# Performance work log

Measured on AMD Instinct MI355X. Metric: run time of the kernel, lower is better.

Reference implementation:

```python
import jax, jax.numpy as jnp
import numpy as np

N = 50000      # nodes
E = 800000     # edges (before self loops)
F_IN = 128     # input feature dim
H = 2          # attention heads
C = 64         # hidden channels per head (H*C = 128 = layer-2 input dim)
G = 64         # graphs in batch
OUT = 10       # out_channels
NEG_SLOPE = 0.2  # PyG GATConv default leaky relu slope


def setup_inputs() -> dict:
    key = jax.random.key(0)
    ks = jax.random.split(key, 16)
    sc = lambda f: np.float32(1.0 / np.sqrt(f))
    inp = {
        "x": jax.random.normal(ks[0], (N, F_IN), jnp.float32),
        "edge_index": jax.random.randint(ks[1], (2, E), 0, N, dtype=jnp.int32),
        "batch": jnp.sort(jax.random.randint(ks[2], (N,), 0, G, dtype=jnp.int32)),
        # GATConv layer 1 (lazy (-1,-1): separate src/dst projections)
        "Ws1": jax.random.normal(ks[3], (F_IN, H * C), jnp.float32) * sc(F_IN),
        "Wd1": jax.random.normal(ks[4], (F_IN, H * C), jnp.float32) * sc(F_IN),
        "as1": jax.random.normal(ks[5], (H, C), jnp.float32) * sc(C),
        "ad1": jax.random.normal(ks[6], (H, C), jnp.float32) * sc(C),
        "b1": jnp.zeros((H * C,), jnp.float32),
        # GATConv layer 2 (input dim = H*C = 128)
        "Ws2": jax.random.normal(ks[7], (H * C, H * C), jnp.float32) * sc(H * C),
        "Wd2": jax.random.normal(ks[8], (H * C, H * C), jnp.float32) * sc(H * C),
        "as2": jax.random.normal(ks[9], (H, C), jnp.float32) * sc(C),
        "ad2": jax.random.normal(ks[10], (H, C), jnp.float32) * sc(C),
        "b2": jnp.zeros((H * C,), jnp.float32),
        # final linear
        "Wl": jax.random.normal(ks[11], (H * C, OUT), jnp.float32) * sc(H * C),
        "bl": jnp.zeros((OUT,), jnp.float32),
    }
    return inp


def gat_conv(x, src, dst, Ws, Wd, att_s, att_d, b):
    # x: [N, F]; src/dst: [E'] (self loops already included)
    n = x.shape[0]
    xs = (x @ Ws).reshape(n, H, C)          # source-side projection
    xd = (x @ Wd).reshape(n, H, C)          # dest-side projection
    a_s = jnp.einsum('nhc,hc->nh', xs, att_s)   # [N, H]
    a_d = jnp.einsum('nhc,hc->nh', xd, att_d)   # [N, H]
    e = a_s[src] + a_d[dst]                      # [E', H]
    e = jnp.where(e > 0, e, NEG_SLOPE * e)       # leaky_relu
    # softmax over incoming edges per destination node (every node has a self loop)
    m = jax.ops.segment_max(e, dst, num_segments=n)
    ew = jnp.exp(e - m[dst])
    denom = jax.ops.segment_sum(ew, dst, num_segments=n)
    alpha = ew / denom[dst]                      # [E', H]
    out = jax.ops.segment_sum(alpha[:, :, None] * xs[src], dst, num_segments=n)
    return out.reshape(n, H * C) + b


def reference(x, edge_index, batch, Ws1, Wd1, as1, ad1, b1, Ws2, Wd2, as2, ad2, b2, Wl, bl):
    # add self loops once (add_self_loops=True)
    loops = jnp.arange(N, dtype=edge_index.dtype)
    src = jnp.concatenate([edge_index[0], loops])
    dst = jnp.concatenate([edge_index[1], loops])

    h = jax.nn.relu(gat_conv(x, src, dst, Ws1, Wd1, as1, ad1, b1))
    h = jax.nn.relu(gat_conv(h, src, dst, Ws2, Wd2, as2, ad2, b2))

    # global_mean_pool over batch vector
    sums = jax.ops.segment_sum(h, batch, num_segments=G)
    cnt = jax.ops.segment_sum(jnp.ones((N,), h.dtype), batch, num_segments=G)
    pooled = sums / jnp.maximum(cnt, 1.0)[:, None]

    # dropout(p=0.5) is identity in eval mode
    return pooled @ Wl + bl
```

## Files before the change

kernel.cpp:

```cpp
#include <hip/hip_runtime.h>
#include <hip/hip_bf16.h>

#define N_NODES 50000
#define N_EDGES 800000
#define EP (N_EDGES + N_NODES)
#define N_GRAPHS 64
#define F_DIM 128
#define OUT_DIM 10
#define NB 391
#define NREP 8
#define SUBCAP 384
#define EIDS_CAP 2560
#define SC_EDGES 4096
#define SC_BLOCKS ((N_EDGES + SC_EDGES - 1) / SC_EDGES)
#define POOL_CHUNK 128
#define POOL_BLOCKS ((N_NODES + POOL_CHUNK - 1) / POOL_CHUNK)

typedef __attribute__((ext_vector_type(8))) short short8;
typedef __attribute__((ext_vector_type(4))) float f32x4;

__device__ __forceinline__ unsigned int f2bf(float f) {
    unsigned int x; __builtin_memcpy(&x, &f, 4);
    return (x + 0x7fffu + ((x >> 16) & 1u)) >> 16;
}
__device__ __forceinline__ float bf2f(unsigned int u16) {
    unsigned int x = u16 << 16;
    float f; __builtin_memcpy(&f, &x, 4); return f;
}


__global__ __launch_bounds__(256) void prep_kernel(
    const float* __restrict__ W1, const float* __restrict__ W2,
    const float* __restrict__ Wd1, const float* __restrict__ ad1,
    const float* __restrict__ Wd2, const float* __restrict__ ad2,
    unsigned short* __restrict__ Wt1, unsigned short* __restrict__ Wt2,
    float* __restrict__ weffd1, float* __restrict__ weffd2,
    uint4* __restrict__ zero_bcur , uint4* __restrict__ zero_sums ) {
    int tid = blockIdx.x * 256 + threadIdx.x;
    if (tid < 782) zero_bcur[tid] = make_uint4(0, 0, 0, 0);
    else if (tid < 782 + 2048) zero_sums[tid - 782] = make_uint4(0, 0, 0, 0);
    if (tid < 512) {
        const float* Wd = (tid < 256) ? Wd1 : Wd2;
        const float* ad = (tid < 256) ? ad1 : ad2;
        float* wout = (tid < 256) ? weffd1 : weffd2;
        int i = tid & 255, f = i >> 1, h = i & 1;
        const float4* wr = (const float4*)(Wd + f * 128 + h * 64);
        const float4* av = (const float4*)(ad + h * 64);
        float s = 0.f;
        #pragma unroll
        for (int c = 0; c < 16; ++c) {
            float4 w = wr[c], a = av[c];
            s += w.x*a.x + w.y*a.y + w.z*a.z + w.w*a.w;
        }
        wout[f * 2 + h] = s;
    }
    const float* W = (tid < 16384) ? W1 : W2;
    unsigned short* Wt = (tid < 16384) ? Wt1 : Wt2;
    int i = tid & 16383;
    int k = i >> 7, nn = i & 127;
    Wt[nn * 128 + k] = (unsigned short)f2bf(W[i]);
}


__global__ __launch_bounds__(1024) void scatter_kernel(const int* __restrict__ ei,
                                                       int* __restrict__ bcursor,
                                                       unsigned int* __restrict__ recs) {
    __shared__ unsigned int srec[SC_EDGES];
    __shared__ int hist[NB], lcur[NB], gpos[NB];
    __shared__ int excl[512];
    int t = threadIdx.x;
    int base = blockIdx.x * SC_EDGES;
    int rep = blockIdx.x & (NREP - 1);
    for (int i = t; i < NB; i += 1024) { hist[i] = 0; lcur[i] = 0; }
    __syncthreads();
    unsigned int rec_[4]; int have[4];
    #pragma unroll
    for (int j = 0; j < 4; ++j) {
        int i = base + j * 1024 + t;
        have[j] = (i < N_EDGES);
        if (have[j]) {
            int src = ei[i], dst = ei[N_EDGES + i];
            int b = dst >> 7;
            rec_[j] = ((unsigned)b << 23) | ((unsigned)(dst & 127) << 16) | (unsigned)src;
            atomicAdd(&hist[b], 1);
        }
    }
    __syncthreads();
    if (t < 512) excl[t] = (t < NB) ? hist[t] : 0;
    __syncthreads();
    for (int off = 1; off < 512; off <<= 1) {
        int v = 0;
        if (t < 512 && t >= off) v = excl[t - off];
        __syncthreads();
        if (t < 512) excl[t] += v;
        __syncthreads();
    }
    if (t < NB && hist[t] > 0) gpos[t] = atomicAdd(&bcursor[rep * NB + t], hist[t]);
    __syncthreads();
    #pragma unroll
    for (int j = 0; j < 4; ++j) {
        if (have[j]) {
            int b = rec_[j] >> 23;
            int pos = atomicAdd(&lcur[b], 1);
            srec[(excl[b] - hist[b]) + pos] = rec_[j];
        }
    }
    __syncthreads();
    int cnt = N_EDGES - base; if (cnt > SC_EDGES) cnt = SC_EDGES;
    for (int i = t; i < cnt; i += 1024) {
        unsigned int rec = srec[i];
        int b = rec >> 23;
        int gp = gpos[b] + (i - (excl[b] - hist[b]));
        if (gp < SUBCAP)
            recs[((size_t)b * NREP + rep) * SUBCAP + gp] = rec & 0x7fffffu;
    }
}

__global__ __launch_bounds__(256) void bucketize_kernel(
    const unsigned int* __restrict__ recs, const int* __restrict__ bcursor,
    unsigned short* __restrict__ eids, int2* __restrict__ rsre, int n) {
    __shared__ int ssub[NREP + 1];
    __shared__ int hist[128], excl[128], cur[128];
    __shared__ unsigned int srec[EIDS_CAP];
    int b = blockIdx.x, t = threadIdx.x;
    int nvalid = n - b * 128; if (nvalid > 128) nvalid = 128;
    if (t < 128) { hist[t] = 0; cur[t] = 0; }
    if (t == 0) {
        int run = 0; ssub[0] = 0;
        for (int r = 0; r < NREP; ++r) {
            int c = bcursor[r * NB + b]; if (c > SUBCAP) c = SUBCAP;
            run += c; ssub[r + 1] = run;
        }
    }
    __syncthreads();
    int total = ssub[NREP];
    int maxsc = EIDS_CAP - 128;
    if (total > maxsc) total = maxsc;
    const unsigned int* rb = recs + (size_t)b * NREP * SUBCAP;
    for (int i = t; i < total; i += 256) {
        int r = 0;
        while (ssub[r + 1] <= i) ++r;
        unsigned int rec = rb[r * SUBCAP + (i - ssub[r])];
        srec[i] = rec;
        atomicAdd(&hist[(rec >> 16) & 127], 1);
    }
    __syncthreads();
    if (t < nvalid) hist[t] += 1;
    __syncthreads();
    if (t < 128) excl[t] = hist[t];
    __syncthreads();
    for (int off = 1; off < 128; off <<= 1) {
        int v = 0;
        if (t < 128 && t >= off) v = excl[t - off];
        __syncthreads();
        if (t < 128) excl[t] += v;
        __syncthreads();
    }
    int base2 = b * EIDS_CAP;
    if (t < nvalid) {
        int st = excl[t] - hist[t];
        rsre[b * 128 + t] = make_int2(base2 + st, base2 + excl[t]);
        eids[base2 + st] = (unsigned short)(b * 128 + t);
        cur[t] = 1;
    }
    __syncthreads();
    for (int i = t; i < total; i += 256) {
        unsigned int rec = srec[i];
        int dl = (rec >> 16) & 127;
        int pos = atomicAdd(&cur[dl], 1);
        eids[base2 + (excl[dl] - hist[dl]) + pos] = (unsigned short)(rec & 0xffffu);
    }
}


__global__ __launch_bounds__(256) void gemm_fused_f32a_kernel(
    const float* __restrict__ A, const unsigned short* __restrict__ Wt,
    const float* __restrict__ att_s, const float* __restrict__ weffd,
    unsigned short* __restrict__ C, float* __restrict__ a_s, float* __restrict__ a_d, int n) {
    int t = threadIdx.x;
    int l = t & 63;
    int quad = l >> 4, lr = l & 15;
    int m0 = blockIdx.x * 64 + (t >> 6) * 16;
    int arow = m0 + lr; if (arow >= n) arow = n - 1;

    short8 afrag[4];
    float pd0 = 0.f, pd1 = 0.f;
    const float2* wd2 = (const float2*)weffd;
    #pragma unroll
    for (int kb = 0; kb < 4; ++kb) {
        const float4* ap = (const float4*)(A + (size_t)arow * 128 + kb * 32 + quad * 8);
        float4 a0 = ap[0], a1 = ap[1];
        int k0 = kb * 32 + quad * 8;
        float2 w0 = wd2[k0+0], w1 = wd2[k0+1], w2 = wd2[k0+2], w3 = wd2[k0+3];
        float2 w4 = wd2[k0+4], w5 = wd2[k0+5], w6 = wd2[k0+6], w7 = wd2[k0+7];
        pd0 += a0.x*w0.x + a0.y*w1.x + a0.z*w2.x + a0.w*w3.x
             + a1.x*w4.x + a1.y*w5.x + a1.z*w6.x + a1.w*w7.x;
        pd1 += a0.x*w0.y + a0.y*w1.y + a0.z*w2.y + a0.w*w3.y
             + a1.x*w4.y + a1.y*w5.y + a1.z*w6.y + a1.w*w7.y;
        short8 s;
        s[0] = (short)f2bf(a0.x); s[1] = (short)f2bf(a0.y);
        s[2] = (short)f2bf(a0.z); s[3] = (short)f2bf(a0.w);
        s[4] = (short)f2bf(a1.x); s[5] = (short)f2bf(a1.y);
        s[6] = (short)f2bf(a1.z); s[7] = (short)f2bf(a1.w);
        afrag[kb] = s;
    }
    pd0 += __shfl_xor(pd0, 16); pd0 += __shfl_xor(pd0, 32);
    pd1 += __shfl_xor(pd1, 16); pd1 += __shfl_xor(pd1, 32);
    if (l < 16 && m0 + lr < n) *(float2*)(a_d + (size_t)(m0 + lr) * 2) = make_float2(pd0, pd1);

    f32x4 acc[8] = {};
    #pragma unroll
    for (int nt = 0; nt < 8; ++nt) {
        #pragma unroll
        for (int kb = 0; kb < 4; ++kb) {
            short8 b = *(const short8*)(Wt + (size_t)(nt * 16 + lr) * 128 + kb * 32 + quad * 8);
            acc[nt] = __builtin_amdgcn_mfma_f32_16x16x32_bf16(afrag[kb], b, acc[nt], 0, 0, 0);
        }
    }
    float asv[8];
    #pragma unroll
    for (int nt = 0; nt < 8; ++nt) asv[nt] = att_s[nt * 16 + lr];
    float pa0[4] = {}, pa1[4] = {};
    #pragma unroll
    for (int nt = 0; nt < 8; ++nt)
        #pragma unroll
        for (int r = 0; r < 4; ++r) {
            if (nt < 4) pa0[r] += acc[nt][r] * asv[nt];
            else        pa1[r] += acc[nt][r] * asv[nt];
        }
    #pragma unroll
    for (int d = 1; d < 16; d <<= 1) {
        #pragma unroll
        for (int r = 0; r < 4; ++r) {
            pa0[r] += __shfl_xor(pa0[r], d);
            pa1[r] += __shfl_xor(pa1[r], d);
        }
    }
    if (lr == 0) {
        #pragma unroll
        for (int r = 0; r < 4; ++r) {
            int row = m0 + quad * 4 + r;
            if (row < n) *(float2*)(a_s + (size_t)row * 2) = make_float2(pa0[r], pa1[r]);
        }
    }
    #pragma unroll
    for (int nt = 0; nt < 8; ++nt)
        #pragma unroll
        for (int r = 0; r < 4; ++r) {
            int row = m0 + quad * 4 + r;
            if (row < n)
                C[(size_t)row * 128 + nt * 16 + lr] = (unsigned short)f2bf(acc[nt][r]);
        }
}

__global__ __launch_bounds__(256) void gemm_fused_bf16_kernel(
    const unsigned short* __restrict__ A, const unsigned short* __restrict__ Wt,
    const float* __restrict__ att_s, const float* __restrict__ weffd,
    unsigned short* __restrict__ C, float* __restrict__ a_s, float* __restrict__ a_d, int n) {
    int t = threadIdx.x;
    int l = t & 63;
    int quad = l >> 4, lr = l & 15;
    int m0 = blockIdx.x * 64 + (t >> 6) * 16;
    int arow = m0 + lr; if (arow >= n) arow = n - 1;

    short8 afrag[4];
    float pd0 = 0.f, pd1 = 0.f;
    const float2* wd2 = (const float2*)weffd;
    #pragma unroll
    for (int kb = 0; kb < 4; ++kb) {
        short8 s = *(const short8*)(A + (size_t)arow * 128 + kb * 32 + quad * 8);
        afrag[kb] = s;
        const unsigned int* u = (const unsigned int*)&s;
        int k0 = kb * 32 + quad * 8;
        #pragma unroll
        for (int d = 0; d < 4; ++d) {
            float x0 = __uint_as_float(u[d] << 16);
            float x1 = __uint_as_float(u[d] & 0xffff0000u);
            float2 wv0 = wd2[k0 + 2*d], wv1 = wd2[k0 + 2*d + 1];
            pd0 += x0 * wv0.x + x1 * wv1.x;
            pd1 += x0 * wv0.y + x1 * wv1.y;
        }
    }
    pd0 += __shfl_xor(pd0, 16); pd0 += __shfl_xor(pd0, 32);
    pd1 += __shfl_xor(pd1, 16); pd1 += __shfl_xor(pd1, 32);
    if (l < 16 && m0 + lr < n) *(float2*)(a_d + (size_t)(m0 + lr) * 2) = make_float2(pd0, pd1);

    f32x4 acc[8] = {};
    #pragma unroll
    for (int nt = 0; nt < 8; ++nt) {
        #pragma unroll
        for (int kb = 0; kb < 4; ++kb) {
            short8 b = *(const short8*)(Wt + (size_t)(nt * 16 + lr) * 128 + kb * 32 + quad * 8);
            acc[nt] = __builtin_amdgcn_mfma_f32_16x16x32_bf16(afrag[kb], b, acc[nt], 0, 0, 0);
        }
    }
    float asv[8];
    #pragma unroll
    for (int nt = 0; nt < 8; ++nt) asv[nt] = att_s[nt * 16 + lr];
    float pa0[4] = {}, pa1[4] = {};
    #pragma unroll
    for (int nt = 0; nt < 8; ++nt)
        #pragma unroll
        for (int r = 0; r < 4; ++r) {
            if (nt < 4) pa0[r] += acc[nt][r] * asv[nt];
            else        pa1[r] += acc[nt][r] * asv[nt];
        }
    #pragma unroll
    for (int d = 1; d < 16; d <<= 1) {
        #pragma unroll
        for (int r = 0; r < 4; ++r) {
            pa0[r] += __shfl_xor(pa0[r], d);
            pa1[r] += __shfl_xor(pa1[r], d);
        }
    }
    if (lr == 0) {
        #pragma unroll
        for (int r = 0; r < 4; ++r) {
            int row = m0 + quad * 4 + r;
            if (row < n) *(float2*)(a_s + (size_t)row * 2) = make_float2(pa0[r], pa1[r]);
        }
    }
    #pragma unroll
    for (int nt = 0; nt < 8; ++nt)
        #pragma unroll
        for (int r = 0; r < 4; ++r) {
            int row = m0 + quad * 4 + r;
            if (row < n)
                C[(size_t)row * 128 + nt * 16 + lr] = (unsigned short)f2bf(acc[nt][r]);
        }
}


#define AGG_GRP(EIV, PME, X0, X1, Y0, Y1, JB)                                   \
    {                                                                           \
        _Pragma("unroll")                                                       \
        for (int u = 0; u < 4; ++u) {                                           \
            int j = (JB) + u;                                                   \
            int srcn = __shfl((EIV), j);                                        \
            float pj = __shfl((PME), j + hoff);                                 \
            unsigned int v = xs32[(size_t)srcn * 64 + lane];                    \
            float v0 = __uint_as_float(v << 16);                                \
            float v1 = __uint_as_float(v & 0xffff0000u);                        \
            if (u & 1) { Y0 += pj * v0; Y1 += pj * v1; }                        \
            else       { X0 += pj * v0; X1 += pj * v1; }                        \
        }                                                                       \
    }

__global__ __launch_bounds__(256) void aggregate_kernel(
    const int2* __restrict__ rsre, const unsigned short* __restrict__ eids,
    const float* __restrict__ a_s, const float* __restrict__ a_d,
    const unsigned int* __restrict__ xs32, const float* __restrict__ bias,
    unsigned int* __restrict__ out32, int npairs) {
    int wv = (int)((blockIdx.x * blockDim.x + threadIdx.x) >> 6);
    int lane = threadIdx.x & 63;
    if (wv >= npairs) return;
    int d0 = wv * 2, d1 = d0 + 1;
    int h = lane >> 5, j32 = lane & 31, hoff = h << 5, ch = lane * 2;
    float2 adp0 = *(const float2*)(a_d + (size_t)d0 * 2);
    float2 adp1 = *(const float2*)(a_d + (size_t)d1 * 2);
    float adv0 = (h == 0) ? adp0.x : adp0.y;
    float adv1 = (h == 0) ? adp1.x : adp1.y;
    int2 r0 = rsre[d0], r1 = rsre[d1];
    int b0 = r0.x, e0 = r0.y, b1 = r1.x, e1 = r1.y;

    float xA0 = 0, xA1 = 0, yA0 = 0, yA1 = 0;
    float xB0 = 0, xB1 = 0, yB0 = 0, yB1 = 0;
    float ls0 = 0, ls1 = 0;
    while (b0 < e0 || b1 < e1) {
        int k0 = e0 - b0; k0 = k0 < 0 ? 0 : (k0 > 32 ? 32 : k0);
        int k1 = e1 - b1; k1 = k1 < 0 ? 0 : (k1 > 32 ? 32 : k1);
        int ei0 = 0, ei1 = 0;
        float pm0 = 0.f, pm1 = 0.f;
        if (k0 > 0) {
            ei0 = (int)eids[b0 + (j32 < k0 ? j32 : k0 - 1)];
            float2 as2 = *(const float2*)(a_s + (size_t)ei0 * 2);
            float ev = ((h == 0) ? as2.x : as2.y) + adv0;
            ev = (ev > 0.f) ? ev : 0.2f * ev;
            pm0 = (j32 < k0) ? __expf(ev) : 0.f;
            ls0 += pm0;
        }
        if (k1 > 0) {
            ei1 = (int)eids[b1 + (j32 < k1 ? j32 : k1 - 1)];
            float2 as2 = *(const float2*)(a_s + (size_t)ei1 * 2);
            float ev = ((h == 0) ? as2.x : as2.y) + adv1;
            ev = (ev > 0.f) ? ev : 0.2f * ev;
            pm1 = (j32 < k1) ? __expf(ev) : 0.f;
            ls1 += pm1;
        }
        int jb0 = 0, jb1 = 0;
        while (jb0 + 4 <= k0 && jb1 + 4 <= k1) {
            AGG_GRP(ei0, pm0, xA0, xA1, yA0, yA1, jb0)
            AGG_GRP(ei1, pm1, xB0, xB1, yB0, yB1, jb1)
            jb0 += 4; jb1 += 4;
        }
        for (; jb0 + 4 <= k0; jb0 += 4) AGG_GRP(ei0, pm0, xA0, xA1, yA0, yA1, jb0)
        for (; jb1 + 4 <= k1; jb1 += 4) AGG_GRP(ei1, pm1, xB0, xB1, yB0, yB1, jb1)
        for (; jb0 < k0; ++jb0) {
            int srcn = __shfl(ei0, jb0);
            float pj = __shfl(pm0, jb0 + hoff);
            unsigned int v = xs32[(size_t)srcn * 64 + lane];
            xA0 += pj * __uint_as_float(v << 16);
            xA1 += pj * __uint_as_float(v & 0xffff0000u);
        }
        for (; jb1 < k1; ++jb1) {
            int srcn = __shfl(ei1, jb1);
            float pj = __shfl(pm1, jb1 + hoff);
            unsigned int v = xs32[(size_t)srcn * 64 + lane];
            xB0 += pj * __uint_as_float(v << 16);
            xB1 += pj * __uint_as_float(v & 0xffff0000u);
        }
        b0 += k0; b1 += k1;
    }
    #pragma unroll
    for (int d = 1; d <= 16; d <<= 1) {
        ls0 += __shfl_xor(ls0, d);
        ls1 += __shfl_xor(ls1, d);
    }
    float inv0 = 1.f / ls0, inv1 = 1.f / ls1;
    float bc0 = bias[ch], bc1 = bias[ch + 1];
    float o00 = fmaxf((xA0 + yA0) * inv0 + bc0, 0.f);
    float o01 = fmaxf((xA1 + yA1) * inv0 + bc1, 0.f);
    float o10 = fmaxf((xB0 + yB0) * inv1 + bc0, 0.f);
    float o11 = fmaxf((xB1 + yB1) * inv1 + bc1, 0.f);
    out32[(size_t)d0 * 64 + lane] = f2bf(o00) | (f2bf(o01) << 16);
    out32[(size_t)d1 * 64 + lane] = f2bf(o10) | (f2bf(o11) << 16);
}


__global__ __launch_bounds__(256) void pool_partial_kernel(
    const unsigned short* __restrict__ Hf, const int* __restrict__ batch,
    float* __restrict__ sums, int n) {
    int t = threadIdx.x;
    int c = t & 127, half = t >> 7;
    int start = blockIdx.x * POOL_CHUNK;
    int end = min(start + POOL_CHUNK, n);
    float acc = 0.f;
    int cur = -1;
    for (int i = start + half; i < end; i += 2) {
        int g = batch[i];
        if (g != cur) {
            if (cur >= 0) atomicAdd(&sums[cur * 128 + c], acc);
            acc = 0.f; cur = g;
        }
        acc += bf2f(Hf[(size_t)i * 128 + c]);
    }
    if (cur >= 0) atomicAdd(&sums[cur * 128 + c], acc);
}

__global__ void final_linear_kernel(const float* __restrict__ sums,
                                    const int* __restrict__ batch,
                                    const float* __restrict__ Wl, const float* __restrict__ bl,
                                    float* __restrict__ out, int n) {
    int t = blockIdx.x * blockDim.x + threadIdx.x;
    if (t >= N_GRAPHS * OUT_DIM) return;
    int g = t / OUT_DIM, o = t % OUT_DIM;
    int lo = 0, hi = n;
    while (lo < hi) { int mid = (lo + hi) >> 1; if (batch[mid] < g) lo = mid + 1; else hi = mid; }
    int s0 = lo; hi = n;
    while (lo < hi) { int mid = (lo + hi) >> 1; if (batch[mid] < g + 1) lo = mid + 1; else hi = mid; }
    float cnt = (float)(lo - s0);
    float inv = 1.f / fmaxf(cnt, 1.f);
    float s = bl[o];
    for (int c = 0; c < 128; ++c) s += sums[g * 128 + c] * inv * Wl[c * OUT_DIM + o];
    out[g * OUT_DIM + o] = s;
}


extern "C" void kernel_launch(void* const* d_in, const int* in_sizes, int n_in,
                              void* d_out, int out_size, void* d_ws, size_t ws_size,
                              hipStream_t stream) {
    const float* x    = (const float*)d_in[0];
    const int*   ei   = (const int*)d_in[1];
    const int*   batch= (const int*)d_in[2];
    const float* Ws1  = (const float*)d_in[3];
    const float* Wd1  = (const float*)d_in[4];
    const float* as1  = (const float*)d_in[5];
    const float* ad1  = (const float*)d_in[6];
    const float* b1   = (const float*)d_in[7];
    const float* Ws2  = (const float*)d_in[8];
    const float* Wd2  = (const float*)d_in[9];
    const float* as2  = (const float*)d_in[10];
    const float* ad2  = (const float*)d_in[11];
    const float* b2   = (const float*)d_in[12];
    const float* Wl   = (const float*)d_in[13];
    const float* bl   = (const float*)d_in[14];
    float* out = (float*)d_out;

    char* p = (char*)d_ws;
    auto alloc = [&](size_t bytes) {
        void* r = (void*)p;
        p += (bytes + 255) & ~(size_t)255;
        return r;
    };
    int* bcursor  = (int*)alloc(sizeof(int) * NREP * NB);
    unsigned short* eids = (unsigned short*)alloc(sizeof(short) * (size_t)NB * EIDS_CAP);
    int2* rsre    = (int2*)alloc(sizeof(int2) * N_NODES);
    float* a_s    = (float*)alloc(sizeof(float) * N_NODES * 2);
    float* a_d    = (float*)alloc(sizeof(float) * N_NODES * 2);
    float* sums   = (float*)alloc(sizeof(float) * N_GRAPHS * 128);
    float* weffd1 = (float*)alloc(sizeof(float) * 128 * 2);
    float* weffd2 = (float*)alloc(sizeof(float) * 128 * 2);
    unsigned short* Wt1  = (unsigned short*)alloc(sizeof(short) * 128 * 128);
    unsigned short* Wt2  = (unsigned short*)alloc(sizeof(short) * 128 * 128);
    unsigned short* bufA = (unsigned short*)alloc(sizeof(short) * (size_t)N_NODES * F_DIM);
    unsigned short* bufB = (unsigned short*)alloc(sizeof(short) * (size_t)N_NODES * F_DIM);
    unsigned int* recs = (unsigned int*)bufA;

    prep_kernel<<<128, 256, 0, stream>>>(Ws1, Ws2, Wd1, ad1, Wd2, ad2,
                                         Wt1, Wt2, weffd1, weffd2,
                                         (uint4*)bcursor, (uint4*)sums);
    scatter_kernel<<<SC_BLOCKS, 1024, 0, stream>>>(ei, bcursor, recs);
    bucketize_kernel<<<NB, 256, 0, stream>>>(recs, bcursor, eids, rsre, N_NODES);

    const int gemm_grid = (N_NODES + 63) / 64;
    const int npairs    = N_NODES / 2;
    const int agg_grid  = (npairs + 3) / 4;

    gemm_fused_f32a_kernel<<<gemm_grid, 256, 0, stream>>>(x, Wt1, as1, weffd1,
                                                          bufA, a_s, a_d, N_NODES);
    aggregate_kernel<<<agg_grid, 256, 0, stream>>>(rsre, eids, a_s, a_d,
                                                   (const unsigned int*)bufA, b1,
                                                   (unsigned int*)bufB, npairs);

    gemm_fused_bf16_kernel<<<gemm_grid, 256, 0, stream>>>(bufB, Wt2, as2, weffd2,
                                                          bufA, a_s, a_d, N_NODES);
    aggregate_kernel<<<agg_grid, 256, 0, stream>>>(rsre, eids, a_s, a_d,
                                                   (const unsigned int*)bufA, b2,
                                                   (unsigned int*)bufB, npairs);

    pool_partial_kernel<<<POOL_BLOCKS, 256, 0, stream>>>(bufB, batch, sums, N_NODES);
    final_linear_kernel<<<(N_GRAPHS * OUT_DIM + 255) / 256, 256, 0, stream>>>(sums, batch, Wl, bl, out, N_NODES);
}
```

Measured before the change: 275.2 us.

## Fuse prep into scatter and bucketize into first GEMM, drop global cursors

Weight prep (transpose to bf16, attention-folded dst weights, zeroing) moves into the edge-scatter kernel. Each scatter block now writes its locally bucket-sorted records plus a per-block exclusive prefix table, instead of using global atomic cursors into replicated sub-buckets. Bucketization runs inside the first GEMM kernel: the first NB blocks gather their bucket's records from all scatter blocks using a prefix scan and binary search, then do the GEMM work. This cuts two kernel launches and the global atomics, at the cost of extra serial work in some GEMM blocks and a larger records buffer.

```diff
diff --git a/kernel.cpp b/kernel.cpp
--- a/kernel.cpp
+++ b/kernel.cpp
@@ -3,13 +3,10 @@
 
 #define N_NODES 50000
 #define N_EDGES 800000
-#define EP (N_EDGES + N_NODES)
 #define N_GRAPHS 64
 #define F_DIM 128
 #define OUT_DIM 10
 #define NB 391
-#define NREP 8
-#define SUBCAP 384
 #define EIDS_CAP 2560
 #define SC_EDGES 4096
 #define SC_BLOCKS ((N_EDGES + SC_EDGES - 1) / SC_EDGES)
@@ -29,21 +26,34 @@
 }
 
 
-__global__ __launch_bounds__(256) void prep_kernel(
+__global__ __launch_bounds__(1024) void scatter_prep_kernel(
+    const int* __restrict__ ei,
     const float* __restrict__ W1, const float* __restrict__ W2,
     const float* __restrict__ Wd1, const float* __restrict__ ad1,
     const float* __restrict__ Wd2, const float* __restrict__ ad2,
     unsigned short* __restrict__ Wt1, unsigned short* __restrict__ Wt2,
     float* __restrict__ weffd1, float* __restrict__ weffd2,
-    uint4* __restrict__ zero_bcur , uint4* __restrict__ zero_sums ) {
-    int tid = blockIdx.x * 256 + threadIdx.x;
-    if (tid < 782) zero_bcur[tid] = make_uint4(0, 0, 0, 0);
-    else if (tid < 782 + 2048) zero_sums[tid - 782] = make_uint4(0, 0, 0, 0);
-    if (tid < 512) {
-        const float* Wd = (tid < 256) ? Wd1 : Wd2;
-        const float* ad = (tid < 256) ? ad1 : ad2;
-        float* wout = (tid < 256) ? weffd1 : weffd2;
-        int i = tid & 255, f = i >> 1, h = i & 1;
+    uint4* __restrict__ zero_sums ,
+    unsigned int* __restrict__ recs, int* __restrict__ exclT) {
+    __shared__ unsigned int srec[SC_EDGES];
+    __shared__ int hist[NB], lcur[NB];
+    __shared__ int excl[512];
+    int t = threadIdx.x;
+    int blk = blockIdx.x;
+    int tid = blk * 1024 + t;
+
+    if (tid < 32768) {
+        const float* W = (tid < 16384) ? W1 : W2;
+        unsigned short* Wt = (tid < 16384) ? Wt1 : Wt2;
+        int i = tid & 16383;
+        int k = i >> 7, nn = i & 127;
+        Wt[nn * 128 + k] = (unsigned short)f2bf(W[i]);
+    } else if (tid < 33280) {
+        int j = tid - 32768;
+        const float* Wd = (j < 256) ? Wd1 : Wd2;
+        const float* ad = (j < 256) ? ad1 : ad2;
+        float* wout = (j < 256) ? weffd1 : weffd2;
+        int i = j & 255, f = i >> 1, h = i & 1;
         const float4* wr = (const float4*)(Wd + f * 128 + h * 64);
         const float4* av = (const float4*)(ad + h * 64);
         float s = 0.f;
@@ -53,24 +63,11 @@
             s += w.x*a.x + w.y*a.y + w.z*a.z + w.w*a.w;
         }
         wout[f * 2 + h] = s;
-    }
-    const float* W = (tid < 16384) ? W1 : W2;
-    unsigned short* Wt = (tid < 16384) ? Wt1 : Wt2;
-    int i = tid & 16383;
-    int k = i >> 7, nn = i & 127;
-    Wt[nn * 128 + k] = (unsigned short)f2bf(W[i]);
-}
-
-
-__global__ __launch_bounds__(1024) void scatter_kernel(const int* __restrict__ ei,
-                                                       int* __restrict__ bcursor,
-                                                       unsigned int* __restrict__ recs) {
-    __shared__ unsigned int srec[SC_EDGES];
-    __shared__ int hist[NB], lcur[NB], gpos[NB];
-    __shared__ int excl[512];
-    int t = threadIdx.x;
-    int base = blockIdx.x * SC_EDGES;
-    int rep = blockIdx.x & (NREP - 1);
+    } else if (tid < 35328) {
+        zero_sums[tid - 33280] = make_uint4(0, 0, 0, 0);
+    }
+
+    int base = blk * SC_EDGES;
     for (int i = t; i < NB; i += 1024) { hist[i] = 0; lcur[i] = 0; }
     __syncthreads();
     unsigned int rec_[4]; int have[4];
@@ -95,8 +92,6 @@
         if (t < 512) excl[t] += v;
         __syncthreads();
     }
-    if (t < NB && hist[t] > 0) gpos[t] = atomicAdd(&bcursor[rep * NB + t], hist[t]);
-    __syncthreads();
     #pragma unroll
     for (int j = 0; j < 4; ++j) {
         if (have[j]) {
@@ -107,77 +102,84 @@
     }
     __syncthreads();
     int cnt = N_EDGES - base; if (cnt > SC_EDGES) cnt = SC_EDGES;
-    for (int i = t; i < cnt; i += 1024) {
-        unsigned int rec = srec[i];
-        int b = rec >> 23;
-        int gp = gpos[b] + (i - (excl[b] - hist[b]));
-        if (gp < SUBCAP)
-            recs[((size_t)b * NREP + rep) * SUBCAP + gp] = rec & 0x7fffffu;
-    }
-}
-
-__global__ __launch_bounds__(256) void bucketize_kernel(
-    const unsigned int* __restrict__ recs, const int* __restrict__ bcursor,
-    unsigned short* __restrict__ eids, int2* __restrict__ rsre, int n) {
-    __shared__ int ssub[NREP + 1];
-    __shared__ int hist[128], excl[128], cur[128];
-    __shared__ unsigned int srec[EIDS_CAP];
-    int b = blockIdx.x, t = threadIdx.x;
-    int nvalid = n - b * 128; if (nvalid > 128) nvalid = 128;
-    if (t < 128) { hist[t] = 0; cur[t] = 0; }
-    if (t == 0) {
-        int run = 0; ssub[0] = 0;
-        for (int r = 0; r < NREP; ++r) {
-            int c = bcursor[r * NB + b]; if (c > SUBCAP) c = SUBCAP;
-            run += c; ssub[r + 1] = run;
-        }
-    }
-    __syncthreads();
-    int total = ssub[NREP];
-    int maxsc = EIDS_CAP - 128;
-    if (total > maxsc) total = maxsc;
-    const unsigned int* rb = recs + (size_t)b * NREP * SUBCAP;
-    for (int i = t; i < total; i += 256) {
-        int r = 0;
-        while (ssub[r + 1] <= i) ++r;
-        unsigned int rec = rb[r * SUBCAP + (i - ssub[r])];
-        srec[i] = rec;
-        atomicAdd(&hist[(rec >> 16) & 127], 1);
-    }
-    __syncthreads();
-    if (t < nvalid) hist[t] += 1;
-    __syncthreads();
-    if (t < 128) excl[t] = hist[t];
-    __syncthreads();
-    for (int off = 1; off < 128; off <<= 1) {
-        int v = 0;
-        if (t < 128 && t >= off) v = excl[t - off];
-        __syncthreads();
-        if (t < 128) excl[t] += v;
-        __syncthreads();
-    }
-    int base2 = b * EIDS_CAP;
-    if (t < nvalid) {
-        int st = excl[t] - hist[t];
-        rsre[b * 128 + t] = make_int2(base2 + st, base2 + excl[t]);
-        eids[base2 + st] = (unsigned short)(b * 128 + t);
-        cur[t] = 1;
-    }
-    __syncthreads();
-    for (int i = t; i < total; i += 256) {
-        unsigned int rec = srec[i];
-        int dl = (rec >> 16) & 127;
-        int pos = atomicAdd(&cur[dl], 1);
-        eids[base2 + (excl[dl] - hist[dl]) + pos] = (unsigned short)(rec & 0xffffu);
-    }
-}
-
-
-__global__ __launch_bounds__(256) void gemm_fused_f32a_kernel(
+    for (int i = t; i < cnt; i += 1024)
+        recs[(size_t)blk * SC_EDGES + i] = srec[i];
+    if (t < NB) exclT[blk * NB + t] = excl[t];
+}
+
+
+__global__ __launch_bounds__(256) void gemm1_bucketize_kernel(
     const float* __restrict__ A, const unsigned short* __restrict__ Wt,
     const float* __restrict__ att_s, const float* __restrict__ weffd,
-    unsigned short* __restrict__ C, float* __restrict__ a_s, float* __restrict__ a_d, int n) {
+    const unsigned int* __restrict__ recs, const int* __restrict__ exclT,
+    unsigned short* __restrict__ C, float* __restrict__ a_s, float* __restrict__ a_d,
+    unsigned short* __restrict__ eids, int2* __restrict__ rsre, int n) {
+    __shared__ unsigned int srec[EIDS_CAP];
+    __shared__ int lo0[SC_BLOCKS], cntb[SC_BLOCKS];
+    __shared__ int sc[256];
+    __shared__ int pexcl[SC_BLOCKS + 1];
+    __shared__ int hist[128], excl[128], cur[128];
     int t = threadIdx.x;
+
+    if (blockIdx.x < NB) {
+        int b = blockIdx.x;
+        int nvalid = n - b * 128; if (nvalid > 128) nvalid = 128;
+        if (t < 128) { hist[t] = 0; cur[t] = 0; }
+        for (int i = t; i < SC_BLOCKS; i += 256) {
+            int hi = exclT[i * NB + b];
+            int l  = b ? exclT[i * NB + b - 1] : 0;
+            lo0[i] = l; cntb[i] = hi - l;
+        }
+        __syncthreads();
+        sc[t] = (t < SC_BLOCKS) ? cntb[t] : 0;
+        __syncthreads();
+        for (int off = 1; off < 256; off <<= 1) {
+            int v = (t >= off) ? sc[t - off] : 0;
+            __syncthreads();
+            sc[t] += v;
+            __syncthreads();
+        }
+        if (t < SC_BLOCKS) pexcl[t] = sc[t] - cntb[t];
+        if (t == 0) pexcl[SC_BLOCKS] = sc[255];
+        __syncthreads();
+        int total = pexcl[SC_BLOCKS];
+        int maxsc = EIDS_CAP - 128;
+        if (total > maxsc) total = maxsc;
+        for (int i = t; i < total; i += 256) {
+            int l = 0, h = SC_BLOCKS;
+            while (l + 1 < h) { int m = (l + h) >> 1; if (pexcl[m] <= i) l = m; else h = m; }
+            unsigned int rec = recs[(size_t)l * SC_EDGES + lo0[l] + (i - pexcl[l])];
+            srec[i] = rec;
+            atomicAdd(&hist[(rec >> 16) & 127], 1);
+        }
+        __syncthreads();
+        if (t < nvalid) hist[t] += 1;
+        __syncthreads();
+        if (t < 128) excl[t] = hist[t];
+        __syncthreads();
+        for (int off = 1; off < 128; off <<= 1) {
+            int v = 0;
+            if (t < 128 && t >= off) v = excl[t - off];
+            __syncthreads();
+            if (t < 128) excl[t] += v;
+            __syncthreads();
+        }
+        int base2 = b * EIDS_CAP;
+        if (t < nvalid) {
+            int st = excl[t] - hist[t];
+            rsre[b * 128 + t] = make_int2(base2 + st, base2 + excl[t]);
+            eids[base2 + st] = (unsigned short)(b * 128 + t);
+            cur[t] = 1;
+        }
+        __syncthreads();
+        for (int i = t; i < total; i += 256) {
+            unsigned int rec = srec[i];
+            int dl = (rec >> 16) & 127;
+            int pos = atomicAdd(&cur[dl], 1);
+            eids[base2 + (excl[dl] - hist[dl]) + pos] = (unsigned short)(rec & 0xffffu);
+        }
+    }
+
     int l = t & 63;
     int quad = l >> 4, lr = l & 15;
     int m0 = blockIdx.x * 64 + (t >> 6) * 16;
@@ -252,6 +254,7 @@
                 C[(size_t)row * 128 + nt * 16 + lr] = (unsigned short)f2bf(acc[nt][r]);
         }
 }
+
 
 __global__ __launch_bounds__(256) void gemm_fused_bf16_kernel(
     const unsigned short* __restrict__ A, const unsigned short* __restrict__ Wt,
@@ -492,7 +495,8 @@
         p += (bytes + 255) & ~(size_t)255;
         return r;
     };
-    int* bcursor  = (int*)alloc(sizeof(int) * NREP * NB);
+    int* exclT    = (int*)alloc(sizeof(int) * SC_BLOCKS * NB);
+    unsigned int* recs = (unsigned int*)alloc(sizeof(int) * (size_t)SC_BLOCKS * SC_EDGES);
     unsigned short* eids = (unsigned short*)alloc(sizeof(short) * (size_t)NB * EIDS_CAP);
     int2* rsre    = (int2*)alloc(sizeof(int2) * N_NODES);
     float* a_s    = (float*)alloc(sizeof(float) * N_NODES * 2);
@@ -504,20 +508,19 @@
     unsigned short* Wt2  = (unsigned short*)alloc(sizeof(short) * 128 * 128);
     unsigned short* bufA = (unsigned short*)alloc(sizeof(short) * (size_t)N_NODES * F_DIM);
     unsigned short* bufB = (unsigned short*)alloc(sizeof(short) * (size_t)N_NODES * F_DIM);
-    unsigned int* recs = (unsigned int*)bufA;
-
-    prep_kernel<<<128, 256, 0, stream>>>(Ws1, Ws2, Wd1, ad1, Wd2, ad2,
-                                         Wt1, Wt2, weffd1, weffd2,
-                                         (uint4*)bcursor, (uint4*)sums);
-    scatter_kernel<<<SC_BLOCKS, 1024, 0, stream>>>(ei, bcursor, recs);
-    bucketize_kernel<<<NB, 256, 0, stream>>>(recs, bcursor, eids, rsre, N_NODES);
 
     const int gemm_grid = (N_NODES + 63) / 64;
     const int npairs    = N_NODES / 2;
     const int agg_grid  = (npairs + 3) / 4;
 
-    gemm_fused_f32a_kernel<<<gemm_grid, 256, 0, stream>>>(x, Wt1, as1, weffd1,
-                                                          bufA, a_s, a_d, N_NODES);
+    scatter_prep_kernel<<<SC_BLOCKS, 1024, 0, stream>>>(ei, Ws1, Ws2, Wd1, ad1, Wd2, ad2,
+                                                        Wt1, Wt2, weffd1, weffd2,
+                                                        (uint4*)sums, recs, exclT);
+
+    gemm1_bucketize_kernel<<<gemm_grid, 256, 0, stream>>>(x, Wt1, as1, weffd1,
+                                                          recs, exclT,
+                                                          bufA, a_s, a_d,
+                                                          eids, rsre, N_NODES);
     aggregate_kernel<<<agg_grid, 256, 0, stream>>>(rsre, eids, a_s, a_d,
                                                    (const unsigned int*)bufA, b1,
                                                    (unsigned int*)bufB, npairs);
```

After: 265.5 us. 1.04x faster.
